# Kernel tuning notes

Measured on AMD Instinct MI355X. Metric: run time of the kernel, lower is better.

## Reference

```python
import jax, jax.numpy as jnp
import numpy as np

N = 50000
E = 800000
IN_DIM, HID, HEADS, OUT_DIM = 32, 64, 4, 128
HC = HID * HEADS  # 256
LN_EPS = 1e-5
NEG_SLOPE = 0.2


def setup_inputs() -> dict:
    key = jax.random.key(0)
    ks = jax.random.split(key, 16)
    s = 0.05
    inp = {
        "x": jax.random.normal(ks[0], (N, IN_DIM), dtype=jnp.float32),
        "edge_index": jax.random.randint(ks[1], (2, E), 0, N, dtype=jnp.int32),
        # input projection
        "W_in": jax.random.normal(ks[2], (IN_DIM, HID), dtype=jnp.float32) * s,
        "b_in": jnp.zeros((HID,), dtype=jnp.float32),
        # GAT layer 0: in=HID, out=HID per head, HEADS heads
        "lin0_w": jax.random.normal(ks[3], (HID, HC), dtype=jnp.float32) * s,
        "att0_src": jax.random.normal(ks[4], (HEADS, HID), dtype=jnp.float32) * s,
        "att0_dst": jax.random.normal(ks[5], (HEADS, HID), dtype=jnp.float32) * s,
        "bias0": jnp.zeros((HC,), dtype=jnp.float32),
        # GAT layer 1: in=HC, out=HID per head
        "lin1_w": jax.random.normal(ks[6], (HC, HC), dtype=jnp.float32) * s,
        "att1_src": jax.random.normal(ks[7], (HEADS, HID), dtype=jnp.float32) * s,
        "att1_dst": jax.random.normal(ks[8], (HEADS, HID), dtype=jnp.float32) * s,
        "bias1": jnp.zeros((HC,), dtype=jnp.float32),
        # output projection + layernorm
        "W_out": jax.random.normal(ks[9], (HC, OUT_DIM), dtype=jnp.float32) * s,
        "b_out": jnp.zeros((OUT_DIM,), dtype=jnp.float32),
        "ln_gamma": jnp.ones((OUT_DIM,), dtype=jnp.float32),
        "ln_beta": jnp.zeros((OUT_DIM,), dtype=jnp.float32),
    }
    return inp


def _gat_conv(x, src, dst, lin_w, att_src, att_dst, bias):
    # x: [N, F_in]; src/dst: [E'] (self-loops included)
    h = (x @ lin_w).reshape(N, HEADS, HID)           # [N, H, C]
    a_src = jnp.einsum("nhc,hc->nh", h, att_src)      # [N, H]
    a_dst = jnp.einsum("nhc,hc->nh", h, att_dst)      # [N, H]
    e = a_src[src] + a_dst[dst]                        # [E', H]
    e = jnp.where(e > 0, e, NEG_SLOPE * e)             # leaky_relu(0.2)
    # segment softmax over incoming edges per destination
    m = jax.ops.segment_max(e, dst, num_segments=N)    # [N, H]
    p = jnp.exp(e - m[dst])
    denom = jax.ops.segment_sum(p, dst, num_segments=N)
    alpha = p / (denom[dst] + 1e-16)                   # [E', H]
    msg = h[src] * alpha[:, :, None]                   # [E', H, C]
    out = jax.ops.segment_sum(msg, dst, num_segments=N)  # [N, H, C]
    return out.reshape(N, HC) + bias


def reference(x, edge_index, W_in, b_in, lin0_w, att0_src, att0_dst, bias0,
              lin1_w, att1_src, att1_dst, bias1, W_out, b_out, ln_gamma, ln_beta):
    # add self-loops (PyG GATConv default)
    loops = jnp.arange(N, dtype=edge_index.dtype)
    src = jnp.concatenate([edge_index[0], loops])
    dst = jnp.concatenate([edge_index[1], loops])

    h = jax.nn.elu(x @ W_in + b_in)
    h = jax.nn.elu(_gat_conv(h, src, dst, lin0_w, att0_src, att0_dst, bias0))
    h = jax.nn.elu(_gat_conv(h, src, dst, lin1_w, att1_src, att1_dst, bias1))
    h = h @ W_out + b_out
    mu = jnp.mean(h, axis=-1, keepdims=True)
    var = jnp.mean((h - mu) ** 2, axis=-1, keepdims=True)
    return (h - mu) * jax.lax.rsqrt(var + LN_EPS) * ln_gamma + ln_beta
```

## Files before the change

### kernel.cpp

```cpp
#include <hip/hip_runtime.h>
#include <cstdint>

#define N_NODES 50000
#define N_EDGES 800000
#define EP (N_EDGES + N_NODES)
#define IN_DIM 32
#define HID 64
#define HEADS 4
#define HC 256
#define OUT_DIM 128
#define NEG_SLOPE 0.2f
#define LN_EPS 1e-5f
#define SCAN_B 1024
#define NB ((N_NODES + SCAN_B - 1) / SCAN_B)

typedef __attribute__((ext_vector_type(8))) short bf16x8;
typedef __attribute__((ext_vector_type(16))) float f32x16;

__device__ __forceinline__ unsigned bf16rne(float f) {
    unsigned u = __float_as_uint(f);
    return (u + 0x7fffu + ((u >> 16) & 1u)) >> 16;
}
__device__ __forceinline__ unsigned pack_bf2(float a, float b) {
    return bf16rne(a) | (bf16rne(b) << 16);
}
__device__ __forceinline__ float bf_lo(unsigned w) { return __uint_as_float(w << 16); }
__device__ __forceinline__ float bf_hi_raw(unsigned w) { return __uint_as_float(w); }

#define PREP_INPROJ ((N_NODES * HID) / 256)
#define PREP_WPACK ((HID * HC + HC * HC + HC * OUT_DIM) / 256)
#define PREP_EXT 40
__global__ void k_prep(const float* __restrict__ x, const float* __restrict__ W_in,
                       const float* __restrict__ b_in, unsigned short* __restrict__ h_in,
                       const float* __restrict__ w0, const float* __restrict__ w1,
                       const float* __restrict__ w2, unsigned short* __restrict__ p0,
                       unsigned short* __restrict__ p1, unsigned short* __restrict__ p2,
                       const float* __restrict__ as0, const float* __restrict__ ad0,
                       unsigned short* __restrict__ ext0,
                       const float* __restrict__ as1, const float* __restrict__ ad1,
                       unsigned short* __restrict__ ext1) {
    if (blockIdx.x < PREP_INPROJ) {
        int g = blockIdx.x * 256 + threadIdx.x;
        int n = g >> 6, j = g & 63;
        const float* xr = x + n * IN_DIM;
        float acc = b_in[j];
#pragma unroll
        for (int k = 0; k < IN_DIM; ++k) acc += xr[k] * W_in[k * HID + j];
        acc = acc > 0.f ? acc : (__expf(acc) - 1.f);
        h_in[g] = (unsigned short)bf16rne(acc);
    } else if (blockIdx.x < PREP_INPROJ + PREP_WPACK) {
        int g = (blockIdx.x - PREP_INPROJ) * 256 + threadIdx.x;
        if (g < HID * HC) {
            int k = g >> 8, n = g & 255;
            p0[(((k >> 3) * HC) + n) * 8 + (k & 7)] = (unsigned short)bf16rne(w0[g]);
        } else if (g < HID * HC + HC * HC) {
            int t = g - HID * HC;
            int k = t >> 8, n = t & 255;
            p1[(((k >> 3) * HC) + n) * 8 + (k & 7)] = (unsigned short)bf16rne(w1[t]);
        } else {
            int t = g - HID * HC - HC * HC;
            int k = t >> 7, n = t & 127;
            p2[(((k >> 3) * OUT_DIM) + n) * 8 + (k & 7)] = (unsigned short)bf16rne(w2[t]);
        }
    } else {
        int t = (blockIdx.x - PREP_INPROJ - PREP_WPACK) * 256 + threadIdx.x;
        const float* w; const float* as; const float* ad; unsigned short* ext; int e;
        if (t < 2048) { w = w0; as = as0; ad = ad0; ext = ext0; e = t; }
        else if (t < 2048 + 8192) { w = w1; as = as1; ad = ad1; ext = ext1; e = t - 2048; }
        else return;
        int kb = e >> 8, rem = e & 255, col = rem >> 3, kk = rem & 7;
        int k = kb * 8 + kk;
        float acc = 0.f;
        if (col < 8) {
            int h = col & 3;
            const float* att = (col < 4) ? as : ad;
#pragma unroll 4
            for (int c = 0; c < HID; ++c) acc += w[k * HC + h * HID + c] * att[h * HID + c];
        }
        ext[e] = (unsigned short)bf16rne(acc);
    }
}

template <int K>
__global__ __launch_bounds__(256) void k_gemm_lin(
        const unsigned short* __restrict__ A, const unsigned short* __restrict__ Bp,
        const unsigned short* __restrict__ Ext, unsigned short* __restrict__ hh,
        float* __restrict__ a_src, float* __restrict__ a_dst) {
    const int lane = threadIdx.x & 63;
    const int quad = lane >> 5, c = lane & 31;
    const int wave = threadIdx.x >> 6;
    const int m0 = blockIdx.x * 64 + (wave >> 1) * 32;
    const int cb = (wave & 1) * 128;
    f32x16 acc[4];
#pragma unroll
    for (int nt = 0; nt < 4; ++nt)
#pragma unroll
        for (int i = 0; i < 16; ++i) acc[nt][i] = 0.f;
    f32x16 acce;
#pragma unroll
    for (int i = 0; i < 16; ++i) acce[i] = 0.f;
    int mrow = m0 + c; if (mrow >= N_NODES) mrow = N_NODES - 1;
    const size_t abase = (size_t)mrow * K + quad * 8;
    for (int k0 = 0; k0 < K; k0 += 16) {
        bf16x8 af = *(const bf16x8*)(A + abase + k0);
        const unsigned short* bk = Bp + ((size_t)(k0 >> 3) + quad) * (HC * 8);
#pragma unroll
        for (int nt = 0; nt < 4; ++nt) {
            bf16x8 bf = *(const bf16x8*)(bk + (cb + nt * 32 + c) * 8);
            acc[nt] = __builtin_amdgcn_mfma_f32_32x32x16_bf16(af, bf, acc[nt], 0, 0, 0);
        }
        if (wave & 1) {
            bf16x8 bfe = *(const bf16x8*)(Ext + ((k0 >> 3) + quad) * 256 + c * 8);
            acce = __builtin_amdgcn_mfma_f32_32x32x16_bf16(af, bfe, acce, 0, 0, 0);
        }
    }
#pragma unroll
    for (int reg = 0; reg < 16; ++reg) {
        int row = (reg & 3) + 8 * (reg >> 2) + 4 * quad;
        int m = m0 + row;
        if (m < N_NODES) {
            size_t base = (size_t)m * HC + cb + c;
#pragma unroll
            for (int nt = 0; nt < 4; ++nt)
                hh[base + nt * 32] = (unsigned short)bf16rne(acc[nt][reg]);
            if ((wave & 1) && c < 8) {
                float v = acce[reg];
                if (c < 4) a_src[m * HEADS + c] = v;
                else       a_dst[m * HEADS + (c - 4)] = v;
            }
        }
    }
}

__global__ void k_hist(const int* __restrict__ ei, int* __restrict__ counts,
                       int* __restrict__ rank) {
    int e = blockIdx.x * blockDim.x + threadIdx.x;
    if (e >= EP) return;
    int d = (e < N_EDGES) ? ei[N_EDGES + e] : (e - N_EDGES);
    rank[e] = atomicAdd(&counts[d], 1);
}

__global__ void k_scan1(const int* __restrict__ counts, int* __restrict__ chunk_excl,
                        int* __restrict__ bsum) {
    __shared__ int buf[SCAN_B];
    int i = blockIdx.x * SCAN_B + threadIdx.x;
    int v = (i < N_NODES) ? counts[i] : 0;
    buf[threadIdx.x] = v;
    __syncthreads();
    for (int off = 1; off < SCAN_B; off <<= 1) {
        int t = (threadIdx.x >= off) ? buf[threadIdx.x - off] : 0;
        __syncthreads();
        buf[threadIdx.x] += t;
        __syncthreads();
    }
    if (i < N_NODES) chunk_excl[i] = buf[threadIdx.x] - v;
    if (threadIdx.x == SCAN_B - 1) bsum[blockIdx.x] = buf[SCAN_B - 1];
}

__global__ void k_scan3(const int* __restrict__ chunk_excl, const int* __restrict__ bsum,
                        int* __restrict__ row_ptr) {
    __shared__ int sbase;
    if (threadIdx.x < 64) {
        int v = (threadIdx.x < blockIdx.x) ? bsum[threadIdx.x] : 0;
#pragma unroll
        for (int mk = 1; mk < 64; mk <<= 1) v += __shfl_xor(v, mk, 64);
        if (threadIdx.x == 0) sbase = v;
    }
    __syncthreads();
    int i = blockIdx.x * SCAN_B + threadIdx.x;
    if (i < N_NODES) row_ptr[i] = chunk_excl[i] + sbase;
    if (i == 0) row_ptr[N_NODES] = EP;
}

__global__ void k_scatter(const int* __restrict__ ei, const int* __restrict__ row_ptr,
                          const int* __restrict__ rank, int* __restrict__ esrc) {
    int e = blockIdx.x * blockDim.x + threadIdx.x;
    if (e >= EP) return;
    int s, d;
    if (e < N_EDGES) { s = ei[e]; d = ei[N_EDGES + e]; } else { s = d = e - N_EDGES; }
    esrc[row_ptr[d] + rank[e]] = s;
}

__global__ __launch_bounds__(256) void k_gat_agg(
        const int* __restrict__ row_ptr, const int* __restrict__ esrc,
        const unsigned short* __restrict__ hh, const float* __restrict__ a_src,
        const float* __restrict__ a_dst, const float* __restrict__ bias,
        unsigned short* __restrict__ out) {
    const int wave = threadIdx.x >> 6;
    const int lane = threadIdx.x & 63;
    const int half = lane >> 5;
    const int l = lane & 31;
    const int d = blockIdx.x * 8 + wave * 2 + half;
    const int h = l >> 3;
    const unsigned c0 = (unsigned)(l * 8);
    const int bsrc = half << 5;
    const float ad = a_dst[((unsigned)d << 2) + h];
    const int beg = row_ptr[d], end = row_ptr[d + 1];
    float acc[8];
#pragma unroll
    for (int t = 0; t < 8; ++t) acc[t] = 0.f;
    float psum = 0.f;
    for (int base = beg; base < end; base += 32) {
        int cnt = end - base; if (cnt > 32) cnt = 32;
        int idx = base + l;
        int myv = esrc[idx < end ? idx : end - 1];
        int i = 0;
        for (; i + 4 <= cnt; i += 4) {
            int s0 = __shfl(myv, bsrc + i, 64);
            int s1 = __shfl(myv, bsrc + i + 1, 64);
            int s2 = __shfl(myv, bsrc + i + 2, 64);
            int s3 = __shfl(myv, bsrc + i + 3, 64);
            float as0 = a_src[((unsigned)s0 << 2) + h];
            float as1 = a_src[((unsigned)s1 << 2) + h];
            float as2 = a_src[((unsigned)s2 << 2) + h];
            float as3 = a_src[((unsigned)s3 << 2) + h];
            uint4 g0 = *(const uint4*)(hh + (((unsigned)s0 << 8) + c0));
            uint4 g1 = *(const uint4*)(hh + (((unsigned)s1 << 8) + c0));
            uint4 g2 = *(const uint4*)(hh + (((unsigned)s2 << 8) + c0));
            uint4 g3 = *(const uint4*)(hh + (((unsigned)s3 << 8) + c0));
            float e0 = as0 + ad, e1 = as1 + ad, e2 = as2 + ad, e3 = as3 + ad;
            e0 = fmaxf(e0, NEG_SLOPE * e0); e1 = fmaxf(e1, NEG_SLOPE * e1);
            e2 = fmaxf(e2, NEG_SLOPE * e2); e3 = fmaxf(e3, NEG_SLOPE * e3);
            float p0 = __expf(e0), p1 = __expf(e1), p2 = __expf(e2), p3 = __expf(e3);
            psum += (p0 + p1) + (p2 + p3);
            acc[0] += p0 * bf_lo(g0.x) + p1 * bf_lo(g1.x) + p2 * bf_lo(g2.x) + p3 * bf_lo(g3.x);
            acc[1] += p0 * bf_hi_raw(g0.x) + p1 * bf_hi_raw(g1.x) + p2 * bf_hi_raw(g2.x) + p3 * bf_hi_raw(g3.x);
            acc[2] += p0 * bf_lo(g0.y) + p1 * bf_lo(g1.y) + p2 * bf_lo(g2.y) + p3 * bf_lo(g3.y);
            acc[3] += p0 * bf_hi_raw(g0.y) + p1 * bf_hi_raw(g1.y) + p2 * bf_hi_raw(g2.y) + p3 * bf_hi_raw(g3.y);
            acc[4] += p0 * bf_lo(g0.z) + p1 * bf_lo(g1.z) + p2 * bf_lo(g2.z) + p3 * bf_lo(g3.z);
            acc[5] += p0 * bf_hi_raw(g0.z) + p1 * bf_hi_raw(g1.z) + p2 * bf_hi_raw(g2.z) + p3 * bf_hi_raw(g3.z);
            acc[6] += p0 * bf_lo(g0.w) + p1 * bf_lo(g1.w) + p2 * bf_lo(g2.w) + p3 * bf_lo(g3.w);
            acc[7] += p0 * bf_hi_raw(g0.w) + p1 * bf_hi_raw(g1.w) + p2 * bf_hi_raw(g2.w) + p3 * bf_hi_raw(g3.w);
        }
        for (; i < cnt; ++i) {
            int s0 = __shfl(myv, bsrc + i, 64);
            float as0 = a_src[((unsigned)s0 << 2) + h];
            uint4 g0 = *(const uint4*)(hh + (((unsigned)s0 << 8) + c0));
            float e0 = as0 + ad;
            e0 = fmaxf(e0, NEG_SLOPE * e0);
            float p0 = __expf(e0);
            psum += p0;
            acc[0] += p0 * bf_lo(g0.x); acc[1] += p0 * bf_hi_raw(g0.x);
            acc[2] += p0 * bf_lo(g0.y); acc[3] += p0 * bf_hi_raw(g0.y);
            acc[4] += p0 * bf_lo(g0.z); acc[5] += p0 * bf_hi_raw(g0.z);
            acc[6] += p0 * bf_lo(g0.w); acc[7] += p0 * bf_hi_raw(g0.w);
        }
    }
    const float inv = 1.f / (psum + 1e-16f);
    const float4 bb0 = *(const float4*)(bias + c0);
    const float4 bb1 = *(const float4*)(bias + c0 + 4);
    float v[8];
    v[0] = acc[0] * inv + bb0.x; v[1] = acc[1] * inv + bb0.y;
    v[2] = acc[2] * inv + bb0.z; v[3] = acc[3] * inv + bb0.w;
    v[4] = acc[4] * inv + bb1.x; v[5] = acc[5] * inv + bb1.y;
    v[6] = acc[6] * inv + bb1.z; v[7] = acc[7] * inv + bb1.w;
#pragma unroll
    for (int t = 0; t < 8; ++t) v[t] = v[t] > 0.f ? v[t] : (__expf(v[t]) - 1.f);
    uint4 pk;
    pk.x = pack_bf2(v[0], v[1]); pk.y = pack_bf2(v[2], v[3]);
    pk.z = pack_bf2(v[4], v[5]); pk.w = pack_bf2(v[6], v[7]);
    *(uint4*)(out + (((size_t)d << 8) + c0)) = pk;
}

__global__ __launch_bounds__(256) void k_gemm_out(
        const unsigned short* __restrict__ A, const unsigned short* __restrict__ Bp,
        const float* __restrict__ b, const float* __restrict__ gamma,
        const float* __restrict__ beta, float* __restrict__ out) {
    const int lane = threadIdx.x & 63;
    const int quad = lane >> 5, c = lane & 31;
    const int m0 = blockIdx.x * 128 + (threadIdx.x >> 6) * 32;
    f32x16 acc[4];
#pragma unroll
    for (int nt = 0; nt < 4; ++nt)
#pragma unroll
        for (int i = 0; i < 16; ++i) acc[nt][i] = 0.f;
    int mrow = m0 + c; if (mrow >= N_NODES) mrow = N_NODES - 1;
    const size_t abase = (size_t)mrow * HC + quad * 8;
    for (int k0 = 0; k0 < HC; k0 += 16) {
        bf16x8 af = *(const bf16x8*)(A + abase + k0);
        const unsigned short* bk = Bp + ((size_t)(k0 >> 3) + quad) * (OUT_DIM * 8);
#pragma unroll
        for (int nt = 0; nt < 4; ++nt) {
            bf16x8 bf = *(const bf16x8*)(bk + (nt * 32 + c) * 8);
            acc[nt] = __builtin_amdgcn_mfma_f32_32x32x16_bf16(af, bf, acc[nt], 0, 0, 0);
        }
    }
    float bb[4], gg[4], be[4];
#pragma unroll
    for (int nt = 0; nt < 4; ++nt) {
        int col = nt * 32 + c;
        bb[nt] = b[col]; gg[nt] = gamma[col]; be[nt] = beta[col];
    }
#pragma unroll
    for (int reg = 0; reg < 16; ++reg) {
        int row = (reg & 3) + 8 * (reg >> 2) + 4 * quad;
        int m = m0 + row;
        float v[4];
        float s = 0.f, s2 = 0.f;
#pragma unroll
        for (int nt = 0; nt < 4; ++nt) {
            v[nt] = acc[nt][reg] + bb[nt];
            s += v[nt]; s2 += v[nt] * v[nt];
        }
#pragma unroll
        for (int mk = 1; mk < 32; mk <<= 1) {
            s += __shfl_xor(s, mk, 64);
            s2 += __shfl_xor(s2, mk, 64);
        }
        float mu = s * (1.f / OUT_DIM);
        float var = s2 * (1.f / OUT_DIM) - mu * mu;
        float inv = rsqrtf(var + LN_EPS);
        if (m < N_NODES) {
            size_t base = (size_t)m * OUT_DIM + c;
#pragma unroll
            for (int nt = 0; nt < 4; ++nt)
                out[base + nt * 32] = (v[nt] - mu) * inv * gg[nt] + be[nt];
        }
    }
}

extern "C" void kernel_launch(void* const* d_in, const int* in_sizes, int n_in,
                              void* d_out, int out_size, void* d_ws, size_t ws_size,
                              hipStream_t stream) {
    const float* x        = (const float*)d_in[0];
    const int*   ei       = (const int*)  d_in[1];
    const float* W_in     = (const float*)d_in[2];
    const float* b_in     = (const float*)d_in[3];
    const float* lin0_w   = (const float*)d_in[4];
    const float* att0_src = (const float*)d_in[5];
    const float* att0_dst = (const float*)d_in[6];
    const float* bias0    = (const float*)d_in[7];
    const float* lin1_w   = (const float*)d_in[8];
    const float* att1_src = (const float*)d_in[9];
    const float* att1_dst = (const float*)d_in[10];
    const float* bias1    = (const float*)d_in[11];
    const float* W_out    = (const float*)d_in[12];
    const float* b_out    = (const float*)d_in[13];
    const float* ln_gamma = (const float*)d_in[14];
    const float* ln_beta  = (const float*)d_in[15];
    float* out = (float*)d_out;

    unsigned short* us = (unsigned short*)d_ws;
    unsigned short* h_in_bf = us;
    unsigned short* hh_bf   = h_in_bf + (size_t)N_NODES * HID;
    unsigned short* feat_bf = hh_bf + (size_t)N_NODES * HC;
    unsigned short* p0      = feat_bf + (size_t)N_NODES * HC;
    unsigned short* p1      = p0 + HID * HC;
    unsigned short* p2      = p1 + HC * HC;
    unsigned short* ext0    = p2 + HC * OUT_DIM;
    unsigned short* ext1    = ext0 + 2048;
    float* a_src = (float*)(ext1 + 8192);
    float* a_dst = a_src + (size_t)N_NODES * HEADS;
    int* counts     = (int*)(a_dst + (size_t)N_NODES * HEADS);
    int* chunk_excl = counts + N_NODES;
    int* bsum       = chunk_excl + N_NODES;
    int* row_ptr    = bsum + NB;
    int* rank       = row_ptr + N_NODES + 1;
    int* esrc       = rank + EP;

    k_prep<<<PREP_INPROJ + PREP_WPACK + PREP_EXT, 256, 0, stream>>>(
        x, W_in, b_in, h_in_bf, lin0_w, lin1_w, W_out, p0, p1, p2,
        att0_src, att0_dst, ext0, att1_src, att1_dst, ext1);

    hipMemsetAsync(counts, 0, N_NODES * sizeof(int), stream);
    k_hist<<<(EP + 255) / 256, 256, 0, stream>>>(ei, counts, rank);
    k_scan1<<<NB, SCAN_B, 0, stream>>>(counts, chunk_excl, bsum);
    k_scan3<<<NB, SCAN_B, 0, stream>>>(chunk_excl, bsum, row_ptr);
    k_scatter<<<(EP + 255) / 256, 256, 0, stream>>>(ei, row_ptr, rank, esrc);

    const int lin_grid = (N_NODES + 63) / 64;
    const int out_grid = (N_NODES + 127) / 128;

    k_gemm_lin<HID><<<lin_grid, 256, 0, stream>>>(h_in_bf, p0, ext0, hh_bf, a_src, a_dst);
    k_gat_agg<<<N_NODES / 8, 256, 0, stream>>>(row_ptr, esrc, hh_bf, a_src, a_dst,
                                               bias0, feat_bf);

    k_gemm_lin<HC><<<lin_grid, 256, 0, stream>>>(feat_bf, p1, ext1, hh_bf, a_src, a_dst);
    k_gat_agg<<<N_NODES / 8, 256, 0, stream>>>(row_ptr, esrc, hh_bf, a_src, a_dst,
                                               bias1, feat_bf);

    k_gemm_out<<<out_grid, 256, 0, stream>>>(feat_bf, p2, b_out, ln_gamma, ln_beta, out);
}
```

Before: 365.0 us.

## Fuse CSR build into prep/GEMM launches and merge scan into one kernel

Folds the histogram pass into the prep kernel, merges the two scan kernels into a single kernel that uses an atomic counter plus spin-wait to collect block sums, and fuses the edge scatter into the first GEMM launch. This cuts the kernel launch count from ten to seven and the per-launch gaps between them. The aggregation kernel also prefetches the next chunk of source indices before processing the current one. The spin-wait in the scan assumes all 49 blocks are co-resident. The scatter pads esrc with zeros so the unconditional prefetch stays in bounds.

```diff
diff --git a/kernel.cpp b/kernel.cpp
--- a/kernel.cpp
+++ b/kernel.cpp
@@ -30,6 +30,7 @@
 #define PREP_INPROJ ((N_NODES * HID) / 256)
 #define PREP_WPACK ((HID * HC + HC * HC + HC * OUT_DIM) / 256)
 #define PREP_EXT 40
+#define PREP_HIST ((EP + 255) / 256)
 __global__ void k_prep(const float* __restrict__ x, const float* __restrict__ W_in,
                        const float* __restrict__ b_in, unsigned short* __restrict__ h_in,
                        const float* __restrict__ w0, const float* __restrict__ w1,
@@ -38,7 +39,9 @@
                        const float* __restrict__ as0, const float* __restrict__ ad0,
                        unsigned short* __restrict__ ext0,
                        const float* __restrict__ as1, const float* __restrict__ ad1,
-                       unsigned short* __restrict__ ext1) {
+                       unsigned short* __restrict__ ext1,
+                       const int* __restrict__ ei, int* __restrict__ counts,
+                       int* __restrict__ rank) {
     if (blockIdx.x < PREP_INPROJ) {
         int g = blockIdx.x * 256 + threadIdx.x;
         int n = g >> 6, j = g & 63;
@@ -62,7 +65,7 @@
             int k = t >> 7, n = t & 127;
             p2[(((k >> 3) * OUT_DIM) + n) * 8 + (k & 7)] = (unsigned short)bf16rne(w2[t]);
         }
-    } else {
+    } else if (blockIdx.x < PREP_INPROJ + PREP_WPACK + PREP_EXT) {
         int t = (blockIdx.x - PREP_INPROJ - PREP_WPACK) * 256 + threadIdx.x;
         const float* w; const float* as; const float* ad; unsigned short* ext; int e;
         if (t < 2048) { w = w0; as = as0; ad = ad0; ext = ext0; e = t; }
@@ -78,71 +81,18 @@
             for (int c = 0; c < HID; ++c) acc += w[k * HC + h * HID + c] * att[h * HID + c];
         }
         ext[e] = (unsigned short)bf16rne(acc);
-    }
-}
-
-template <int K>
-__global__ __launch_bounds__(256) void k_gemm_lin(
-        const unsigned short* __restrict__ A, const unsigned short* __restrict__ Bp,
-        const unsigned short* __restrict__ Ext, unsigned short* __restrict__ hh,
-        float* __restrict__ a_src, float* __restrict__ a_dst) {
-    const int lane = threadIdx.x & 63;
-    const int quad = lane >> 5, c = lane & 31;
-    const int wave = threadIdx.x >> 6;
-    const int m0 = blockIdx.x * 64 + (wave >> 1) * 32;
-    const int cb = (wave & 1) * 128;
-    f32x16 acc[4];
-#pragma unroll
-    for (int nt = 0; nt < 4; ++nt)
-#pragma unroll
-        for (int i = 0; i < 16; ++i) acc[nt][i] = 0.f;
-    f32x16 acce;
-#pragma unroll
-    for (int i = 0; i < 16; ++i) acce[i] = 0.f;
-    int mrow = m0 + c; if (mrow >= N_NODES) mrow = N_NODES - 1;
-    const size_t abase = (size_t)mrow * K + quad * 8;
-    for (int k0 = 0; k0 < K; k0 += 16) {
-        bf16x8 af = *(const bf16x8*)(A + abase + k0);
-        const unsigned short* bk = Bp + ((size_t)(k0 >> 3) + quad) * (HC * 8);
-#pragma unroll
-        for (int nt = 0; nt < 4; ++nt) {
-            bf16x8 bf = *(const bf16x8*)(bk + (cb + nt * 32 + c) * 8);
-            acc[nt] = __builtin_amdgcn_mfma_f32_32x32x16_bf16(af, bf, acc[nt], 0, 0, 0);
-        }
-        if (wave & 1) {
-            bf16x8 bfe = *(const bf16x8*)(Ext + ((k0 >> 3) + quad) * 256 + c * 8);
-            acce = __builtin_amdgcn_mfma_f32_32x32x16_bf16(af, bfe, acce, 0, 0, 0);
-        }
-    }
-#pragma unroll
-    for (int reg = 0; reg < 16; ++reg) {
-        int row = (reg & 3) + 8 * (reg >> 2) + 4 * quad;
-        int m = m0 + row;
-        if (m < N_NODES) {
-            size_t base = (size_t)m * HC + cb + c;
-#pragma unroll
-            for (int nt = 0; nt < 4; ++nt)
-                hh[base + nt * 32] = (unsigned short)bf16rne(acc[nt][reg]);
-            if ((wave & 1) && c < 8) {
-                float v = acce[reg];
-                if (c < 4) a_src[m * HEADS + c] = v;
-                else       a_dst[m * HEADS + (c - 4)] = v;
-            }
-        }
-    }
-}
-
-__global__ void k_hist(const int* __restrict__ ei, int* __restrict__ counts,
-                       int* __restrict__ rank) {
-    int e = blockIdx.x * blockDim.x + threadIdx.x;
-    if (e >= EP) return;
-    int d = (e < N_EDGES) ? ei[N_EDGES + e] : (e - N_EDGES);
-    rank[e] = atomicAdd(&counts[d], 1);
-}
-
-__global__ void k_scan1(const int* __restrict__ counts, int* __restrict__ chunk_excl,
-                        int* __restrict__ bsum) {
+    } else {
+        int e = (blockIdx.x - PREP_INPROJ - PREP_WPACK - PREP_EXT) * 256 + threadIdx.x;
+        if (e >= EP) return;
+        int d = (e < N_EDGES) ? ei[N_EDGES + e] : (e - N_EDGES);
+        rank[e] = atomicAdd(&counts[d], 1);
+    }
+}
+
+__global__ void k_scan(const int* __restrict__ counts, int* __restrict__ bsum,
+                       int* __restrict__ done, int* __restrict__ row_ptr) {
     __shared__ int buf[SCAN_B];
+    __shared__ int sbase;
     int i = blockIdx.x * SCAN_B + threadIdx.x;
     int v = (i < N_NODES) ? counts[i] : 0;
     buf[threadIdx.x] = v;
@@ -153,32 +103,109 @@
         buf[threadIdx.x] += t;
         __syncthreads();
     }
-    if (i < N_NODES) chunk_excl[i] = buf[threadIdx.x] - v;
-    if (threadIdx.x == SCAN_B - 1) bsum[blockIdx.x] = buf[SCAN_B - 1];
-}
-
-__global__ void k_scan3(const int* __restrict__ chunk_excl, const int* __restrict__ bsum,
-                        int* __restrict__ row_ptr) {
-    __shared__ int sbase;
+    int excl = buf[threadIdx.x] - v;
+    if (threadIdx.x == SCAN_B - 1) {
+        bsum[blockIdx.x] = buf[SCAN_B - 1];
+        __threadfence();
+        atomicAdd(done, 1);
+    }
+    if (threadIdx.x == 0) {
+        while (__hip_atomic_load(done, __ATOMIC_RELAXED, __HIP_MEMORY_SCOPE_AGENT) < NB) {
+            __builtin_amdgcn_s_sleep(8);
+        }
+    }
+    __syncthreads();
     if (threadIdx.x < 64) {
-        int v = (threadIdx.x < blockIdx.x) ? bsum[threadIdx.x] : 0;
-#pragma unroll
-        for (int mk = 1; mk < 64; mk <<= 1) v += __shfl_xor(v, mk, 64);
-        if (threadIdx.x == 0) sbase = v;
+        int t = threadIdx.x;
+        int val = (t < blockIdx.x)
+                ? __hip_atomic_load(&bsum[t], __ATOMIC_RELAXED, __HIP_MEMORY_SCOPE_AGENT) : 0;
+#pragma unroll
+        for (int mk = 1; mk < 64; mk <<= 1) val += __shfl_xor(val, mk, 64);
+        if (t == 0) sbase = val;
     }
     __syncthreads();
-    int i = blockIdx.x * SCAN_B + threadIdx.x;
-    if (i < N_NODES) row_ptr[i] = chunk_excl[i] + sbase;
+    if (i < N_NODES) row_ptr[i] = excl + sbase;
     if (i == 0) row_ptr[N_NODES] = EP;
 }
 
-__global__ void k_scatter(const int* __restrict__ ei, const int* __restrict__ row_ptr,
-                          const int* __restrict__ rank, int* __restrict__ esrc) {
-    int e = blockIdx.x * blockDim.x + threadIdx.x;
-    if (e >= EP) return;
-    int s, d;
-    if (e < N_EDGES) { s = ei[e]; d = ei[N_EDGES + e]; } else { s = d = e - N_EDGES; }
-    esrc[row_ptr[d] + rank[e]] = s;
+template <int K>
+__device__ __forceinline__ void gemm_lin_body(
+        int mblk, const unsigned short* __restrict__ A, const unsigned short* __restrict__ Bp,
+        const unsigned short* __restrict__ Ext, unsigned short* __restrict__ hh,
+        float* __restrict__ a_src, float* __restrict__ a_dst) {
+    const int lane = threadIdx.x & 63;
+    const int quad = lane >> 5, c = lane & 31;
+    const int wave = threadIdx.x >> 6;
+    const int m0 = mblk * 64 + (wave >> 1) * 32;
+    const int cb = (wave & 1) * 128;
+    f32x16 acc[4];
+#pragma unroll
+    for (int nt = 0; nt < 4; ++nt)
+#pragma unroll
+        for (int i = 0; i < 16; ++i) acc[nt][i] = 0.f;
+    f32x16 acce;
+#pragma unroll
+    for (int i = 0; i < 16; ++i) acce[i] = 0.f;
+    int mrow = m0 + c; if (mrow >= N_NODES) mrow = N_NODES - 1;
+    const size_t abase = (size_t)mrow * K + quad * 8;
+    for (int k0 = 0; k0 < K; k0 += 16) {
+        bf16x8 af = *(const bf16x8*)(A + abase + k0);
+        const unsigned short* bk = Bp + ((size_t)(k0 >> 3) + quad) * (HC * 8);
+#pragma unroll
+        for (int nt = 0; nt < 4; ++nt) {
+            bf16x8 bf = *(const bf16x8*)(bk + (cb + nt * 32 + c) * 8);
+            acc[nt] = __builtin_amdgcn_mfma_f32_32x32x16_bf16(af, bf, acc[nt], 0, 0, 0);
+        }
+        if (wave & 1) {
+            bf16x8 bfe = *(const bf16x8*)(Ext + ((k0 >> 3) + quad) * 256 + c * 8);
+            acce = __builtin_amdgcn_mfma_f32_32x32x16_bf16(af, bfe, acce, 0, 0, 0);
+        }
+    }
+#pragma unroll
+    for (int reg = 0; reg < 16; ++reg) {
+        int row = (reg & 3) + 8 * (reg >> 2) + 4 * quad;
+        int m = m0 + row;
+        if (m < N_NODES) {
+            size_t base = (size_t)m * HC + cb + c;
+#pragma unroll
+            for (int nt = 0; nt < 4; ++nt)
+                hh[base + nt * 32] = (unsigned short)bf16rne(acc[nt][reg]);
+            if ((wave & 1) && c < 8) {
+                float v = acce[reg];
+                if (c < 4) a_src[m * HEADS + c] = v;
+                else       a_dst[m * HEADS + (c - 4)] = v;
+            }
+        }
+    }
+}
+
+template <int K>
+__global__ __launch_bounds__(256) void k_gemm_lin(
+        const unsigned short* __restrict__ A, const unsigned short* __restrict__ Bp,
+        const unsigned short* __restrict__ Ext, unsigned short* __restrict__ hh,
+        float* __restrict__ a_src, float* __restrict__ a_dst) {
+    gemm_lin_body<K>(blockIdx.x, A, Bp, Ext, hh, a_src, a_dst);
+}
+
+#define G0_BLOCKS ((N_NODES + 63) / 64)
+__global__ __launch_bounds__(256) void k_gemm0_scatter(
+        const unsigned short* __restrict__ A, const unsigned short* __restrict__ Bp,
+        const unsigned short* __restrict__ Ext, unsigned short* __restrict__ hh,
+        float* __restrict__ a_src, float* __restrict__ a_dst,
+        const int* __restrict__ ei, const int* __restrict__ row_ptr,
+        const int* __restrict__ rank, int* __restrict__ esrc) {
+    if (blockIdx.x < G0_BLOCKS) {
+        gemm_lin_body<HID>(blockIdx.x, A, Bp, Ext, hh, a_src, a_dst);
+        return;
+    }
+    int e = (blockIdx.x - G0_BLOCKS) * 256 + threadIdx.x;
+    if (e < EP) {
+        int s, d;
+        if (e < N_EDGES) { s = ei[e]; d = ei[N_EDGES + e]; } else { s = d = e - N_EDGES; }
+        esrc[row_ptr[d] + rank[e]] = s;
+    } else if (e - EP < 64) {
+        esrc[e] = 0;
+    }
 }
 
 __global__ __launch_bounds__(256) void k_gat_agg(
@@ -200,10 +227,12 @@
 #pragma unroll
     for (int t = 0; t < 8; ++t) acc[t] = 0.f;
     float psum = 0.f;
+    int myv = esrc[beg + l];
     for (int base = beg; base < end; base += 32) {
-        int cnt = end - base; if (cnt > 32) cnt = 32;
-        int idx = base + l;
-        int myv = esrc[idx < end ? idx : end - 1];
+        int rem = end - base;
+        int cnt = rem > 32 ? 32 : rem;
+        int nxt = 0;
+        if (rem > 32) nxt = esrc[base + 32 + l];
         int i = 0;
         for (; i + 4 <= cnt; i += 4) {
             int s0 = __shfl(myv, bsrc + i, 64);
@@ -245,6 +274,7 @@
             acc[4] += p0 * bf_lo(g0.z); acc[5] += p0 * bf_hi_raw(g0.z);
             acc[6] += p0 * bf_lo(g0.w); acc[7] += p0 * bf_hi_raw(g0.w);
         }
+        myv = nxt;
     }
     const float inv = 1.f / (psum + 1e-16f);
     const float4 bb0 = *(const float4*)(bias + c0);
@@ -351,33 +381,31 @@
     unsigned short* ext1    = ext0 + 2048;
     float* a_src = (float*)(ext1 + 8192);
     float* a_dst = a_src + (size_t)N_NODES * HEADS;
-    int* counts     = (int*)(a_dst + (size_t)N_NODES * HEADS);
-    int* chunk_excl = counts + N_NODES;
-    int* bsum       = chunk_excl + N_NODES;
-    int* row_ptr    = bsum + NB;
-    int* rank       = row_ptr + N_NODES + 1;
-    int* esrc       = rank + EP;
-
-    k_prep<<<PREP_INPROJ + PREP_WPACK + PREP_EXT, 256, 0, stream>>>(
+    int* counts  = (int*)(a_dst + (size_t)N_NODES * HEADS);
+    int* done    = counts + N_NODES;
+    int* bsum    = done + 1;
+    int* row_ptr = bsum + NB;
+    int* rank    = row_ptr + N_NODES + 1;
+    int* esrc    = rank + EP;
+
+    hipMemsetAsync(counts, 0, (N_NODES + 1) * sizeof(int), stream);
+
+    k_prep<<<PREP_INPROJ + PREP_WPACK + PREP_EXT + PREP_HIST, 256, 0, stream>>>(
         x, W_in, b_in, h_in_bf, lin0_w, lin1_w, W_out, p0, p1, p2,
-        att0_src, att0_dst, ext0, att1_src, att1_dst, ext1);
-
-    hipMemsetAsync(counts, 0, N_NODES * sizeof(int), stream);
-    k_hist<<<(EP + 255) / 256, 256, 0, stream>>>(ei, counts, rank);
-    k_scan1<<<NB, SCAN_B, 0, stream>>>(counts, chunk_excl, bsum);
-    k_scan3<<<NB, SCAN_B, 0, stream>>>(chunk_excl, bsum, row_ptr);
-    k_scatter<<<(EP + 255) / 256, 256, 0, stream>>>(ei, row_ptr, rank, esrc);
-
-    const int lin_grid = (N_NODES + 63) / 64;
-    const int out_grid = (N_NODES + 127) / 128;
-
-    k_gemm_lin<HID><<<lin_grid, 256, 0, stream>>>(h_in_bf, p0, ext0, hh_bf, a_src, a_dst);
+        att0_src, att0_dst, ext0, att1_src, att1_dst, ext1, ei, counts, rank);
+
+    k_scan<<<NB, SCAN_B, 0, stream>>>(counts, bsum, done, row_ptr);
+
+    k_gemm0_scatter<<<G0_BLOCKS + PREP_HIST, 256, 0, stream>>>(
+        h_in_bf, p0, ext0, hh_bf, a_src, a_dst, ei, row_ptr, rank, esrc);
     k_gat_agg<<<N_NODES / 8, 256, 0, stream>>>(row_ptr, esrc, hh_bf, a_src, a_dst,
                                                bias0, feat_bf);
 
-    k_gemm_lin<HC><<<lin_grid, 256, 0, stream>>>(feat_bf, p1, ext1, hh_bf, a_src, a_dst);
+    k_gemm_lin<HC><<<(N_NODES + 63) / 64, 256, 0, stream>>>(feat_bf, p1, ext1, hh_bf,
+                                                            a_src, a_dst);
     k_gat_agg<<<N_NODES / 8, 256, 0, stream>>>(row_ptr, esrc, hh_bf, a_src, a_dst,
                                                bias1, feat_bf);
 
-    k_gemm_out<<<out_grid, 256, 0, stream>>>(feat_bf, p2, b_out, ln_gamma, ln_beta, out);
-}
+    k_gemm_out<<<(N_NODES + 127) / 128, 256, 0, stream>>>(feat_bf, p2, b_out,
+                                                          ln_gamma, ln_beta, out);
+}
```

New measurement: 357.7 us. -2.0%, faster.
